# Optimization experiments

Measured on AMD Instinct MI355X. Metric: run time of the kernel, lower is better.

Reference implementation:

```python
import jax, jax.numpy as jnp
import numpy as np

B, T, C, R = 4, 2048, 2048, 256


def setup_inputs() -> dict:
    key = jax.random.key(0)
    ks = jax.random.split(key, 12)
    s = 0.02
    return {
        "x": jax.random.normal(ks[0], (B, T, C), dtype=jnp.float32),
        "h_state": jnp.zeros((B, C), dtype=jnp.float32),
        "ln_gamma": jnp.ones((C,), dtype=jnp.float32),
        "ln_beta": jnp.zeros((C,), dtype=jnp.float32),
        "wq_a": jax.random.normal(ks[1], (C, R), dtype=jnp.float32) * s,
        "wq_b": jax.random.normal(ks[2], (R, C), dtype=jnp.float32) * s,
        "wk_a": jax.random.normal(ks[3], (C, R), dtype=jnp.float32) * s,
        "wk_b": jax.random.normal(ks[4], (R, C), dtype=jnp.float32) * s,
        "wv_a": jax.random.normal(ks[5], (C, R), dtype=jnp.float32) * s,
        "wv_b": jax.random.normal(ks[6], (R, C), dtype=jnp.float32) * s,
        "out_w": jax.random.normal(ks[7], (C, C), dtype=jnp.float32) * s,
        "out_b": jnp.zeros((C,), dtype=jnp.float32),
        "time_decay": jnp.full((C,), -0.5, dtype=jnp.float32),
    }


def _layernorm(x, gamma, beta, eps=1e-5):
    mu = jnp.mean(x, axis=-1, keepdims=True)
    var = jnp.var(x, axis=-1, keepdims=True)
    return (x - mu) * jax.lax.rsqrt(var + eps) * gamma + beta


def reference(x, h_state, ln_gamma, ln_beta, wq_a, wq_b, wk_a, wk_b, wv_a, wv_b, out_w, out_b, time_decay):
    b, t, c = x.shape
    xn = _layernorm(x, ln_gamma, ln_beta)
    # token shift: mix current with previous token
    x_shift = jnp.concatenate([jnp.zeros((b, 1, c), xn.dtype), xn[:, :-1, :]], axis=1)
    mix = 0.5 * xn + 0.5 * x_shift
    # low-rank projections: (B,T,C) @ (C,R) @ (R,C)
    q = jnp.einsum('btc,cr,rd->btd', mix, wq_a, wq_b)
    k = jnp.einsum('btc,cr,rd->btd', mix, wk_a, wk_b)
    v = jnp.einsum('btc,cr,rd->btd', mix, wv_a, wv_b)
    decay = jnp.exp(-jnp.exp(time_decay))  # (C,)

    kv = (k * v).transpose(1, 0, 2)          # (T,B,C)
    sq = jax.nn.sigmoid(q).transpose(1, 0, 2)  # (T,B,C)

    def step(h, inp):
        kv_t, sq_t = inp
        h = decay * h + kv_t
        return h, sq_t * h

    h_final, ys = jax.lax.scan(step, h_state, (kv, sq))
    out = ys.transpose(1, 0, 2)               # (B,T,C)
    out = jnp.einsum('btc,dc->btd', out, out_w) + out_b
    return out, h_final
```

## Files before the change

kernel.cpp:

```cpp
#include <hip/hip_runtime.h>


typedef __attribute__((ext_vector_type(8))) __bf16 bf16x8;
typedef __attribute__((ext_vector_type(4))) float f32x4;

static constexpr int Bb = 4, Tt = 2048, Cc = 2048, Rr = 256;
static constexpr int Mrows = Bb * Tt;
static constexpr int NCH = 32, CLEN = 64;

__device__ __forceinline__ unsigned short f2bf(float f) {
  union { float f; unsigned u; } a; a.f = f;
  unsigned r = (a.u + 0x7FFFu + ((a.u >> 16) & 1u)) >> 16;
  return (unsigned short)r;
}
__device__ __forceinline__ float bf2f(unsigned short h) {
  union { unsigned u; float f; } a; a.u = ((unsigned)h) << 16;
  return a.f;
}

__device__ __forceinline__ void gload16(const void* g, void* l) {
  __builtin_amdgcn_global_load_lds(
      (const __attribute__((address_space(1))) void*)g,
      (__attribute__((address_space(3))) void*)l, 16, 0, 0);
}

__global__ void prep_weights(const float* __restrict__ wqa, const float* __restrict__ wka,
                             const float* __restrict__ wva, const float* __restrict__ wqb,
                             const float* __restrict__ wkb, const float* __restrict__ wvb,
                             const float* __restrict__ ow,  const float* __restrict__ td,
                             unsigned short* __restrict__ waT, unsigned short* __restrict__ wbT,
                             unsigned short* __restrict__ owT, float* __restrict__ decay,
                             float* __restrict__ decayL) {
  const int g = blockIdx.x * blockDim.x + threadIdx.x;
  const int stride = gridDim.x * blockDim.x;
  for (int i = g; i < 3 * Rr * Cc; i += stride) {
    int c = i & (Cc - 1); int jj = i >> 11; int p = jj >> 8; int r = jj & (Rr - 1);
    const float* w = (p == 0) ? wqa : ((p == 1) ? wka : wva);
    waT[i] = f2bf(w[(size_t)c * Rr + r]);
  }
  for (int i = g; i < 3 * Cc * Rr; i += stride) {
    int r = i & (Rr - 1); int d = (i >> 8) & (Cc - 1); int p = i >> 19;
    const float* w = (p == 0) ? wqb : ((p == 1) ? wkb : wvb);
    wbT[i] = f2bf(w[(size_t)r * Cc + d]);
  }
  for (int i = g; i < Cc * Cc; i += stride) owT[i] = f2bf(ow[i]);
  for (int i = g; i < Cc; i += stride) {
    float e = expf(td[i]);
    decay[i] = expf(-e);
    decayL[i] = expf(-(float)CLEN * e);
  }
}

__global__ void ln_stats_kernel(const float* __restrict__ x, float* __restrict__ stats) {
  const int row = blockIdx.x;
  const float* xr = x + (size_t)row * Cc;
  float sum = 0.f, sq = 0.f;
  for (int i = threadIdx.x; i < Cc / 4; i += 256) {
    float4 v = ((const float4*)xr)[i];
    sum += v.x + v.y + v.z + v.w;
    sq  += v.x * v.x + v.y * v.y + v.z * v.z + v.w * v.w;
  }
  for (int off = 32; off; off >>= 1) {
    sum += __shfl_down(sum, off);
    sq  += __shfl_down(sq, off);
  }
  __shared__ float s[8];
  if ((threadIdx.x & 63) == 0) { s[(threadIdx.x >> 6) * 2] = sum; s[(threadIdx.x >> 6) * 2 + 1] = sq; }
  __syncthreads();
  if (threadIdx.x == 0) {
    float ts = 0.f, tq = 0.f;
    for (int wv = 0; wv < 4; ++wv) { ts += s[wv * 2]; tq += s[wv * 2 + 1]; }
    float mean = ts * (1.0f / Cc);
    float var  = tq * (1.0f / Cc) - mean * mean;
    stats[row * 2] = mean;
    stats[row * 2 + 1] = rsqrtf(var + 1e-5f);
  }
}

__global__ void mix_kernel(const float* __restrict__ x, const float* __restrict__ stats,
                           const float* __restrict__ gamma, const float* __restrict__ beta,
                           unsigned short* __restrict__ mix) {
  const int total4 = Mrows * (Cc / 4);
  for (int i = blockIdx.x * blockDim.x + threadIdx.x; i < total4; i += gridDim.x * blockDim.x) {
    const int c4 = i & (Cc / 4 - 1);
    const int m  = i >> 9;
    const int t  = m & (Tt - 1);
    const float4 xv = ((const float4*)x)[i];
    const float mu = stats[2 * m], rs = stats[2 * m + 1];
    const float4 g  = ((const float4*)gamma)[c4];
    const float4 bb = ((const float4*)beta)[c4];
    float mx = (xv.x - mu) * rs * g.x + bb.x;
    float my = (xv.y - mu) * rs * g.y + bb.y;
    float mz = (xv.z - mu) * rs * g.z + bb.z;
    float mw = (xv.w - mu) * rs * g.w + bb.w;
    if (t > 0) {
      const float4 pv = ((const float4*)x)[i - Cc / 4];
      const float pmu = stats[2 * (m - 1)], prs = stats[2 * (m - 1) + 1];
      mx = 0.5f * (mx + (pv.x - pmu) * prs * g.x + bb.x);
      my = 0.5f * (my + (pv.y - pmu) * prs * g.y + bb.y);
      mz = 0.5f * (mz + (pv.z - pmu) * prs * g.z + bb.z);
      mw = 0.5f * (mw + (pv.w - pmu) * prs * g.w + bb.w);
    } else {
      mx *= 0.5f; my *= 0.5f; mz *= 0.5f; mw *= 0.5f;
    }
    ushort4 o;
    o.x = f2bf(mx); o.y = f2bf(my); o.z = f2bf(mz); o.w = f2bf(mw);
    ((ushort4*)mix)[i] = o;
  }
}

template <bool STORE_BF16, bool ADD_BIAS>
__global__ __launch_bounds__(256, 2) void gemm_tile(
    const unsigned short* __restrict__ A, int lda,
    const unsigned short* __restrict__ Bt, int ldb,
    void* __restrict__ Cout, int ldc, int K,
    const float* __restrict__ bias) {
  __shared__ unsigned short As[128 * 64];
  __shared__ unsigned short Bs[128 * 64];
  const int tid = threadIdx.x;
  const int lane = tid & 63;
  const int w = tid >> 6;
  const int wr = w >> 1, wc = w & 1;
  const int fr = lane & 15, fq = lane >> 4;
  const long n0 = (long)blockIdx.x * 128;
  const long m0 = (long)blockIdx.y * 128;

  f32x4 acc[4][4];
#pragma unroll
  for (int i = 0; i < 4; ++i)
#pragma unroll
    for (int j = 0; j < 4; ++j) acc[i][j] = (f32x4){0.f, 0.f, 0.f, 0.f};

  const int srow = tid >> 3;
  const int scol = (tid & 7) * 8;
  const unsigned short* Ag = A + (m0 + srow) * (long)lda + scol;
  const unsigned short* Bg = Bt + (n0 + srow) * (long)ldb + scol;

  for (int kt = 0; kt < K; kt += 64) {
#pragma unroll
    for (int r = 0; r < 4; ++r) {
      gload16(Ag + (long)(r * 32) * lda + kt, &As[r * 2048 + tid * 8]);
      gload16(Bg + (long)(r * 32) * ldb + kt, &Bs[r * 2048 + tid * 8]);
    }
    __syncthreads();
#pragma unroll
    for (int kk = 0; kk < 64; kk += 32) {
      bf16x8 af[4], bfr[4];
#pragma unroll
      for (int i = 0; i < 4; ++i) af[i] = *(const bf16x8*)&As[(wr * 64 + i * 16 + fr) * 64 + kk + fq * 8];
#pragma unroll
      for (int j = 0; j < 4; ++j) bfr[j] = *(const bf16x8*)&Bs[(wc * 64 + j * 16 + fr) * 64 + kk + fq * 8];
#pragma unroll
      for (int i = 0; i < 4; ++i)
#pragma unroll
        for (int j = 0; j < 4; ++j)
          acc[i][j] = __builtin_amdgcn_mfma_f32_16x16x32_bf16(af[i], bfr[j], acc[i][j], 0, 0, 0);
    }
    __syncthreads();
  }

#pragma unroll
  for (int j = 0; j < 4; ++j) {
    const long col = n0 + wc * 64 + j * 16 + fr;
    const float bv = ADD_BIAS ? bias[col] : 0.0f;
#pragma unroll
    for (int i = 0; i < 4; ++i) {
      const long row0 = m0 + wr * 64 + i * 16 + fq * 4;
#pragma unroll
      for (int r = 0; r < 4; ++r) {
        float val = acc[i][j][r] + bv;
        if (STORE_BF16)
          ((unsigned short*)Cout)[(row0 + r) * ldc + col] = f2bf(val);
        else
          ((float*)Cout)[(row0 + r) * ldc + col] = val;
      }
    }
  }
}

template <bool STORE_BF16, bool ADD_BIAS>
__global__ __launch_bounds__(512, 2) void gemm_pipe(
    const unsigned short* __restrict__ A0p, long lda, long aStrideP,
    const unsigned short* __restrict__ B0p, long ldb, long bStrideP,
    void* c0, void* c1, void* c2, long ldc, int K,
    const float* __restrict__ bias, int nbx, int nby) {
  __shared__ unsigned short lds[4 * 16384];
  const int tid = threadIdx.x;
  const int nwg = gridDim.x;
  const int id = blockIdx.x;
  const int q = nwg >> 3;
  const int swz = (id & 7) * q + (id >> 3);
  const int per = nbx * nby;
  const int p = swz / per;
  const int r2 = swz - p * per;
  const int mblk = r2 / nbx;
  const int nblk = r2 - mblk * nbx;
  const unsigned short* A  = A0p + (long)p * aStrideP;
  const unsigned short* Bt = B0p + (long)p * bStrideP;
  void* Cout = (p == 0) ? c0 : (p == 1 ? c1 : c2);
  const long m0 = (long)mblk * 256, n0 = (long)nblk * 256;

  const int lane = tid & 63, wid = tid >> 6;
  const int wm = wid >> 2, wn = wid & 3;
  const int fr = lane & 15, fq = lane >> 4;

  const int srow = tid >> 2;
  const int scolE = (tid & 3) * 8;
  const unsigned short* Ag = A + (m0 + srow) * lda + scolE;
  const unsigned short* Bg = Bt + (n0 + srow) * ldb + scolE;

  const unsigned short* aBase = &lds[(wm * 128 + fr) * 32 + fq * 8];
  const unsigned short* bBase = &lds[8192 + (wn * 64 + fr) * 32 + fq * 8];

  f32x4 acc[8][4];
#pragma unroll
  for (int i = 0; i < 8; ++i)
#pragma unroll
    for (int j = 0; j < 4; ++j) acc[i][j] = (f32x4){0.f, 0.f, 0.f, 0.f};

  const int NT = K >> 5;

  auto stageA = [&](int t) {
    unsigned short* d = &lds[(t & 3) * 16384 + tid * 8];
    const long kt = (long)t * 32;
    gload16(Ag + kt, d);
    gload16(Ag + 128 * lda + kt, d + 4096);
  };
  auto stageB = [&](int t) {
    unsigned short* d = &lds[(t & 3) * 16384 + 8192 + tid * 8];
    const long kt = (long)t * 32;
    gload16(Bg + kt, d);
    gload16(Bg + 128 * ldb + kt, d + 4096);
  };

  stageA(0); stageB(0);
  stageA(1); stageB(1);
  stageA(2); stageB(2);

  for (int t = 0; t < NT; ++t) {
    const int rem = NT - 1 - t;
    if (rem >= 2)      asm volatile("s_waitcnt vmcnt(8)" ::: "memory");
    else if (rem == 1) asm volatile("s_waitcnt vmcnt(4)" ::: "memory");
    else               asm volatile("s_waitcnt vmcnt(0)" ::: "memory");
    __builtin_amdgcn_s_barrier();

    const unsigned short* ab = aBase + (t & 3) * 16384;
    const unsigned short* bb = bBase + (t & 3) * 16384;

    bf16x8 bf[4];
#pragma unroll
    for (int j = 0; j < 4; ++j) bf[j] = *(const bf16x8*)(bb + j * 512);
    bf16x8 af[4];
#pragma unroll
    for (int i = 0; i < 4; ++i) af[i] = *(const bf16x8*)(ab + i * 512);
    if (t + 3 < NT) stageA(t + 3);
    __builtin_amdgcn_s_barrier();
    __builtin_amdgcn_s_setprio(1);
#pragma unroll
    for (int i = 0; i < 4; ++i)
#pragma unroll
      for (int j = 0; j < 4; ++j)
        acc[i][j] = __builtin_amdgcn_mfma_f32_16x16x32_bf16(af[i], bf[j], acc[i][j], 0, 0, 0);
    __builtin_amdgcn_s_setprio(0);
    __builtin_amdgcn_s_barrier();

#pragma unroll
    for (int i = 0; i < 4; ++i) af[i] = *(const bf16x8*)(ab + (4 + i) * 512);
    if (t + 3 < NT) stageB(t + 3);
    __builtin_amdgcn_s_barrier();
    __builtin_amdgcn_s_setprio(1);
#pragma unroll
    for (int i = 0; i < 4; ++i)
#pragma unroll
      for (int j = 0; j < 4; ++j)
        acc[4 + i][j] = __builtin_amdgcn_mfma_f32_16x16x32_bf16(af[i], bf[j], acc[4 + i][j], 0, 0, 0);
    __builtin_amdgcn_s_setprio(0);
  }

#pragma unroll
  for (int j = 0; j < 4; ++j) {
    const long col = n0 + wn * 64 + j * 16 + fr;
    const float bv = ADD_BIAS ? bias[col] : 0.0f;
#pragma unroll
    for (int i = 0; i < 8; ++i) {
      const long row0 = m0 + wm * 128 + i * 16 + fq * 4;
#pragma unroll
      for (int r = 0; r < 4; ++r) {
        float val = acc[i][j][r] + bv;
        if (STORE_BF16)
          ((unsigned short*)Cout)[(row0 + r) * ldc + col] = f2bf(val);
        else
          ((float*)Cout)[(row0 + r) * ldc + col] = val;
      }
    }
  }
}

__global__ void scan_phaseA(const unsigned short* __restrict__ k, const unsigned short* __restrict__ v,
                            const float* __restrict__ decay, float* __restrict__ hend) {
  const int g = blockIdx.x * 256 + threadIdx.x;
  const int c = g & (Cc - 1);
  const int j = (g >> 11) & (NCH - 1);
  const int b = g >> 16;
  const float d = decay[c];
  size_t base = ((size_t)(b * Tt + j * CLEN)) * Cc + c;
  float h = 0.f;
#pragma unroll 8
  for (int s = 0; s < CLEN; ++s) {
    size_t idx = base + (size_t)s * Cc;
    float kv = bf2f(k[idx]) * bf2f(v[idx]);
    h = fmaf(d, h, kv);
  }
  hend[(size_t)(b * NCH + j) * Cc + c] = h;
}

__global__ void scan_combine(const float* __restrict__ hend, const float* __restrict__ h0,
                             const float* __restrict__ decayL, float* __restrict__ Hin,
                             float* __restrict__ hfinal) {
  const int g = blockIdx.x * 256 + threadIdx.x;
  const int c = g & (Cc - 1);
  float H = h0[g];
  const float dl = decayL[c];
  const int b = g >> 11;
  for (int j = 0; j < NCH; ++j) {
    size_t idx = (size_t)(b * NCH + j) * Cc + c;
    Hin[idx] = H;
    H = fmaf(dl, H, hend[idx]);
  }
  hfinal[g] = H;
}

__global__ void scan_phaseB(const unsigned short* __restrict__ q, const unsigned short* __restrict__ k,
                            const unsigned short* __restrict__ v, const float* __restrict__ decay,
                            const float* __restrict__ Hin, unsigned short* __restrict__ ys) {
  const int g = blockIdx.x * 256 + threadIdx.x;
  const int c = g & (Cc - 1);
  const int j = (g >> 11) & (NCH - 1);
  const int b = g >> 16;
  const float d = decay[c];
  float h = Hin[(size_t)(b * NCH + j) * Cc + c];
  size_t base = ((size_t)(b * Tt + j * CLEN)) * Cc + c;
#pragma unroll 4
  for (int s = 0; s < CLEN; ++s) {
    size_t idx = base + (size_t)s * Cc;
    float kv = bf2f(k[idx]) * bf2f(v[idx]);
    h = fmaf(d, h, kv);
    float qq = bf2f(q[idx]);
    float sg = 1.f / (1.f + expf(-qq));
    ys[idx] = f2bf(sg * h);
  }
}

extern "C" void kernel_launch(void* const* d_in, const int* in_sizes, int n_in,
                              void* d_out, int out_size, void* d_ws, size_t ws_size,
                              hipStream_t stream) {
  const float* x   = (const float*)d_in[0];
  const float* h0  = (const float*)d_in[1];
  const float* gam = (const float*)d_in[2];
  const float* bet = (const float*)d_in[3];
  const float* wqa = (const float*)d_in[4];
  const float* wqb = (const float*)d_in[5];
  const float* wka = (const float*)d_in[6];
  const float* wkb = (const float*)d_in[7];
  const float* wva = (const float*)d_in[8];
  const float* wvb = (const float*)d_in[9];
  const float* ow  = (const float*)d_in[10];
  const float* ob  = (const float*)d_in[11];
  const float* td  = (const float*)d_in[12];
  float* out = (float*)d_out;

  char* ws = (char*)d_ws;
  unsigned short* waT   = (unsigned short*)(ws + 0);
  unsigned short* wbT   = (unsigned short*)(ws + 3145728);
  unsigned short* owT   = (unsigned short*)(ws + 6291456);
  float*          decay = (float*)(ws + 14680064);
  float*          decayL= (float*)(ws + 14688256);
  float*          stats = (float*)(ws + 14696448);
  unsigned short* mixb  = (unsigned short*)(ws + 14761984);
  unsigned short* tmp   = (unsigned short*)(ws + 48316416);
  unsigned short* vp    = (unsigned short*)(ws + 60899328);
  float*          hend  = (float*)(ws + 94453760);
  float*          Hin   = (float*)(ws + 95502336);
  unsigned short* qp = (unsigned short*)d_out;
  unsigned short* kp = qp + (size_t)Mrows * Cc;
  float* hfinal = out + (size_t)Mrows * Cc;
  unsigned short* ysb = mixb;

  prep_weights<<<1024, 256, 0, stream>>>(wqa, wka, wva, wqb, wkb, wvb, ow, td,
                                         waT, wbT, owT, decay, decayL);
  ln_stats_kernel<<<Mrows, 256, 0, stream>>>(x, stats);
  mix_kernel<<<2048, 256, 0, stream>>>(x, stats, gam, bet, mixb);

  gemm_tile<true, false><<<dim3(768 / 128, Mrows / 128), 256, 0, stream>>>(
      mixb, Cc, waT, Cc, tmp, 768, Cc, nullptr);

  gemm_pipe<true, false><<<8 * 32 * 3, 512, 0, stream>>>(
      tmp, 768, 256, wbT, Rr, (long)Cc * Rr,
      qp, kp, vp, Cc, Rr, nullptr, 8, 32);

  scan_phaseA<<<(Bb * NCH * Cc) / 256, 256, 0, stream>>>(kp, vp, decay, hend);
  scan_combine<<<(Bb * Cc) / 256, 256, 0, stream>>>(hend, h0, decayL, Hin, hfinal);
  scan_phaseB<<<(Bb * NCH * Cc) / 256, 256, 0, stream>>>(qp, kp, vp, decay, Hin, ysb);

  gemm_pipe<false, true><<<8 * 32, 512, 0, stream>>>(
      ysb, Cc, 0, owT, Cc, 0,
      out, out, out, Cc, Cc, ob, 8, 32);
}
```

Before: 274.4 us.

## Swizzle LDS layout in pipelined GEMM and use it for first projection

Adds an XOR swizzle to the LDS staging and fragment-read addresses in the pipelined GEMM to avoid bank conflicts. It also replaces the simple 128x128 tile GEMM for the rank-768 down-projection with the 256x256 multi-stage pipelined GEMM, launched as 96 workgroups. The larger tiles reuse data better and overlap loads with compute, but 96 workgroups may underfill the GPU's compute units.

```diff
diff --git a/kernel.cpp b/kernel.cpp
--- a/kernel.cpp
+++ b/kernel.cpp
@@ -110,75 +110,6 @@
 }
 
 template <bool STORE_BF16, bool ADD_BIAS>
-__global__ __launch_bounds__(256, 2) void gemm_tile(
-    const unsigned short* __restrict__ A, int lda,
-    const unsigned short* __restrict__ Bt, int ldb,
-    void* __restrict__ Cout, int ldc, int K,
-    const float* __restrict__ bias) {
-  __shared__ unsigned short As[128 * 64];
-  __shared__ unsigned short Bs[128 * 64];
-  const int tid = threadIdx.x;
-  const int lane = tid & 63;
-  const int w = tid >> 6;
-  const int wr = w >> 1, wc = w & 1;
-  const int fr = lane & 15, fq = lane >> 4;
-  const long n0 = (long)blockIdx.x * 128;
-  const long m0 = (long)blockIdx.y * 128;
-
-  f32x4 acc[4][4];
-#pragma unroll
-  for (int i = 0; i < 4; ++i)
-#pragma unroll
-    for (int j = 0; j < 4; ++j) acc[i][j] = (f32x4){0.f, 0.f, 0.f, 0.f};
-
-  const int srow = tid >> 3;
-  const int scol = (tid & 7) * 8;
-  const unsigned short* Ag = A + (m0 + srow) * (long)lda + scol;
-  const unsigned short* Bg = Bt + (n0 + srow) * (long)ldb + scol;
-
-  for (int kt = 0; kt < K; kt += 64) {
-#pragma unroll
-    for (int r = 0; r < 4; ++r) {
-      gload16(Ag + (long)(r * 32) * lda + kt, &As[r * 2048 + tid * 8]);
-      gload16(Bg + (long)(r * 32) * ldb + kt, &Bs[r * 2048 + tid * 8]);
-    }
-    __syncthreads();
-#pragma unroll
-    for (int kk = 0; kk < 64; kk += 32) {
-      bf16x8 af[4], bfr[4];
-#pragma unroll
-      for (int i = 0; i < 4; ++i) af[i] = *(const bf16x8*)&As[(wr * 64 + i * 16 + fr) * 64 + kk + fq * 8];
-#pragma unroll
-      for (int j = 0; j < 4; ++j) bfr[j] = *(const bf16x8*)&Bs[(wc * 64 + j * 16 + fr) * 64 + kk + fq * 8];
-#pragma unroll
-      for (int i = 0; i < 4; ++i)
-#pragma unroll
-        for (int j = 0; j < 4; ++j)
-          acc[i][j] = __builtin_amdgcn_mfma_f32_16x16x32_bf16(af[i], bfr[j], acc[i][j], 0, 0, 0);
-    }
-    __syncthreads();
-  }
-
-#pragma unroll
-  for (int j = 0; j < 4; ++j) {
-    const long col = n0 + wc * 64 + j * 16 + fr;
-    const float bv = ADD_BIAS ? bias[col] : 0.0f;
-#pragma unroll
-    for (int i = 0; i < 4; ++i) {
-      const long row0 = m0 + wr * 64 + i * 16 + fq * 4;
-#pragma unroll
-      for (int r = 0; r < 4; ++r) {
-        float val = acc[i][j][r] + bv;
-        if (STORE_BF16)
-          ((unsigned short*)Cout)[(row0 + r) * ldc + col] = f2bf(val);
-        else
-          ((float*)Cout)[(row0 + r) * ldc + col] = val;
-      }
-    }
-  }
-}
-
-template <bool STORE_BF16, bool ADD_BIAS>
 __global__ __launch_bounds__(512, 2) void gemm_pipe(
     const unsigned short* __restrict__ A0p, long lda, long aStrideP,
     const unsigned short* __restrict__ B0p, long ldb, long bStrideP,
@@ -205,12 +136,13 @@
   const int fr = lane & 15, fq = lane >> 4;
 
   const int srow = tid >> 2;
-  const int scolE = (tid & 3) * 8;
-  const unsigned short* Ag = A + (m0 + srow) * lda + scolE;
-  const unsigned short* Bg = Bt + (n0 + srow) * ldb + scolE;
-
-  const unsigned short* aBase = &lds[(wm * 128 + fr) * 32 + fq * 8];
-  const unsigned short* bBase = &lds[8192 + (wn * 64 + fr) * 32 + fq * 8];
+  const int s_src = (tid & 3) ^ ((tid >> 3) & 3);
+  const unsigned short* Ag = A + (m0 + srow) * lda + s_src * 8;
+  const unsigned short* Bg = Bt + (n0 + srow) * ldb + s_src * 8;
+
+  const int swzs = fq ^ ((fr >> 1) & 3);
+  const unsigned short* aBase = &lds[(wm * 128 + fr) * 32 + swzs * 8];
+  const unsigned short* bBase = &lds[8192 + (wn * 64 + fr) * 32 + swzs * 8];
 
   f32x4 acc[8][4];
 #pragma unroll
@@ -391,8 +323,9 @@
   ln_stats_kernel<<<Mrows, 256, 0, stream>>>(x, stats);
   mix_kernel<<<2048, 256, 0, stream>>>(x, stats, gam, bet, mixb);
 
-  gemm_tile<true, false><<<dim3(768 / 128, Mrows / 128), 256, 0, stream>>>(
-      mixb, Cc, waT, Cc, tmp, 768, Cc, nullptr);
+  gemm_pipe<true, false><<<96, 512, 0, stream>>>(
+      mixb, Cc, 0, waT, Cc, 0,
+      tmp, tmp, tmp, 768, Cc, nullptr, 3, 32);
 
   gemm_pipe<true, false><<<8 * 32 * 3, 512, 0, stream>>>(
       tmp, 768, 256, wbT, Rr, (long)Cc * Rr,
```

Result: slower. 280.5 us (+2.2%).
